# Kernel tuning notes

Measured on AMD Instinct MI355X. Metric: run time of the kernel, lower is better.

Reference implementation:

```python
import jax, jax.numpy as jnp
import numpy as np
from jax import lax

B_BLK = 16   # block size B
N_Z = 64     # latent dim


def setup_inputs() -> dict:
    key = jax.random.key(0)
    ks = jax.random.split(key, 6)
    in_ch, out_ch = 256, 256
    L = (out_ch // B_BLK) * (in_ch // B_BLK)  # 256 latent codes
    x = jax.random.normal(ks[0], (32, in_ch, 64, 64), dtype=jnp.float32)
    z = jax.random.normal(ks[1], (L, N_Z), dtype=jnp.float32)
    W1 = jax.random.normal(ks[2], (B_BLK, N_Z, N_Z), dtype=jnp.float32) * 0.1
    B1 = jax.random.normal(ks[3], (B_BLK, N_Z), dtype=jnp.float32) * 0.1
    W2 = jax.random.normal(ks[4], (B_BLK, B_BLK * 9, N_Z), dtype=jnp.float32) * 0.1
    B2 = jax.random.normal(ks[5], (B_BLK, B_BLK * 9), dtype=jnp.float32) * 0.1
    return {"x": x, "z": z, "W1": W1, "B1": B1, "W2": W2, "B2": B2}


def _aggregate_weight(z, W1, B1, W2, B2, out_ch, in_ch):
    # hypertype='separate', batched over all L = (out_ch//B)*(in_ch//B) blocks.
    # per block: a = W1 @ z + B1 -> (B, N_z); K = W2 @ a[...,None] + B2 -> (B, B*9)
    a = jnp.einsum('bdn,ln->lbd', W1, z) + B1            # (L, B, N_z)
    K = jnp.einsum('bkd,lbd->lbk', W2, a) + B2           # (L, B, B*9)
    ob, ib = out_ch // B_BLK, in_ch // B_BLK
    K = K.reshape(ob, ib, B_BLK, B_BLK, 3, 3)            # (o_blk, i_blk, b1, b2, 3, 3)
    # torch: K.reshape(B,B,3,3).permute(1,0,2,3) => weight_block[p,q] = K[q,p]
    # then cat over i_blk on dim 1 (in), over o_blk on dim 0 (out)
    w = K.transpose(0, 3, 1, 2, 4, 5)                    # (o_blk, b2, i_blk, b1, 3, 3)
    return w.reshape(out_ch, in_ch, 3, 3)


def reference(x, z, W1, B1, W2, B2):
    out_ch, in_ch = 256, 256
    weight = _aggregate_weight(z, W1, B1, W2, B2, out_ch, in_ch)
    # F.conv2d(x, weight, bias=None, stride=1, padding=kernel_size//2=1)
    return lax.conv_general_dilated(
        x, weight,
        window_strides=(1, 1),
        padding=[(1, 1), (1, 1)],
        dimension_numbers=('NCHW', 'OIHW', 'NCHW'))
```

## Files before the change

kernel.cpp:

```cpp
#include <hip/hip_runtime.h>

typedef unsigned short u16;
typedef unsigned int u32;
typedef __attribute__((ext_vector_type(8))) short short8;
typedef __attribute__((ext_vector_type(4))) float f32x4;

__device__ __forceinline__ u16 f2bf(float f) {
    u32 u = __float_as_uint(f);
    return (u16)((u + 0x7FFFu + ((u >> 16) & 1u)) >> 16);
}

#define COMP(f4, e) ((e) == 0 ? (f4).x : (e) == 1 ? (f4).y : (e) == 2 ? (f4).z : (f4).w)

__device__ __forceinline__ void gld16(const u16* g, u16* l) {
    __builtin_amdgcn_global_load_lds(
        (const __attribute__((address_space(1))) unsigned int*)(unsigned long long)(const void*)g,
        (__attribute__((address_space(3))) unsigned int*)(unsigned long long)(void*)l,
        16, 0, 0);
}

__global__ __launch_bounds__(256) void nchw2nhwc_pad(const float* __restrict__ x,
                                                     u16* __restrict__ xp) {
    __shared__ __align__(16) u16 T[64][264];
    const int tid = threadIdx.x;
    const int b   = blockIdx.x;
    const int n   = b >> 6;
    const int row = b & 63;
    const int g16 = tid >> 4;
    const int pxq = tid & 15;

    const float* src = x + ((size_t)n * 256 + g16 * 16) * 4096 + row * 64 + pxq * 4;
    float4 v[4][4];
#pragma unroll
    for (int u = 0; u < 4; ++u)
#pragma unroll
        for (int i = 0; i < 4; ++i)
            v[u][i] = *(const float4*)(src + (size_t)(u * 4 + i) * 4096);

#pragma unroll
    for (int u = 0; u < 4; ++u) {
        const int ic = g16 * 16 + u * 4;
#pragma unroll
        for (int e = 0; e < 4; ++e) {
            const int px = pxq * 4 + e;
            const u32 lo = ((u32)f2bf(COMP(v[u][1], e)) << 16) | f2bf(COMP(v[u][0], e));
            const u32 hi = ((u32)f2bf(COMP(v[u][3], e)) << 16) | f2bf(COMP(v[u][2], e));
            *(uint2*)&T[px][ic] = make_uint2(lo, hi);
        }
    }
    __syncthreads();

    const int c = tid & 31, p0 = tid >> 5;
    u16* dstN = xp + ((size_t)n * 4356 + (size_t)(row + 1) * 66 + 1) * 256 + c * 8;
#pragma unroll
    for (int pp = 0; pp < 8; ++pp) {
        const int px = pp * 8 + p0;
        *(uint4*)(dstN + (size_t)px * 256) = *(const uint4*)&T[px][c * 8];
    }

    u16* hrow = xp + ((size_t)n * 4356 + (size_t)(row + 1) * 66) * 256;
    if (tid < 64) {
        const int wp = (tid >> 5) ? 65 : 0;
        uint4 zz = {0u, 0u, 0u, 0u};
        *(uint4*)(hrow + (size_t)wp * 256 + (tid & 31) * 8) = zz;
    }
    if (row == 0) {
        u16* tb = xp + (size_t)n * 4356 * 256;
        uint4 zz = {0u, 0u, 0u, 0u};
        for (int i = tid; i < 2112; i += 256) *(uint4*)(tb + (size_t)i * 8) = zz;
    }
    if (row == 63) {
        u16* bb = xp + ((size_t)n * 4356 + 65 * 66) * 256;
        uint4 zz = {0u, 0u, 0u, 0u};
        for (int i = tid; i < 2112; i += 256) *(uint4*)(bb + (size_t)i * 8) = zz;
    }
}

__global__ __launch_bounds__(256) void wgen(const float* __restrict__ z,
                                            const float* __restrict__ W1,
                                            const float* __restrict__ B1,
                                            const float* __restrict__ W2,
                                            const float* __restrict__ B2,
                                            u16* __restrict__ wb) {
    __shared__ float zl[64][65];
    __shared__ float w1s[4096];
    __shared__ float aS[64][65];
    __shared__ float w2s[9216];

    const int tid = threadIdx.x;
    const int b   = blockIdx.x >> 2;
    const int lc  = blockIdx.x & 3;
    const int l   = tid & 63;
    const int g   = tid >> 6;

    const float* zg  = z  + (size_t)lc * 4096;
    const float* w1g = W1 + (size_t)b * 4096;
    const float* w2g = W2 + (size_t)b * 9216;
#pragma unroll
    for (int k = 0; k < 4; ++k) {
        const int i4 = tid + k * 256;
        const float4 v = *(const float4*)(zg + (size_t)i4 * 4);
        const int lr = i4 >> 4, nr = (i4 * 4) & 63;
        zl[lr][nr] = v.x; zl[lr][nr + 1] = v.y; zl[lr][nr + 2] = v.z; zl[lr][nr + 3] = v.w;
        *(float4*)(w1s + (size_t)i4 * 4) = *(const float4*)(w1g + (size_t)i4 * 4);
    }
#pragma unroll
    for (int k = 0; k < 9; ++k) {
        const int i4 = tid + k * 256;
        *(float4*)(w2s + (size_t)i4 * 4) = *(const float4*)(w2g + (size_t)i4 * 4);
    }
    __syncthreads();

    {
        float acc[16];
#pragma unroll
        for (int j = 0; j < 16; ++j) acc[j] = B1[b * 64 + g * 16 + j];
#pragma unroll
        for (int nb = 0; nb < 16; ++nb) {
            float zv0 = zl[l][nb * 4 + 0];
            float zv1 = zl[l][nb * 4 + 1];
            float zv2 = zl[l][nb * 4 + 2];
            float zv3 = zl[l][nb * 4 + 3];
#pragma unroll
            for (int j = 0; j < 16; ++j) {
                const float4 w = *(const float4*)(w1s + (g * 16 + j) * 64 + nb * 4);
                acc[j] += w.x * zv0 + w.y * zv1 + w.z * zv2 + w.w * zv3;
            }
        }
#pragma unroll
        for (int j = 0; j < 16; ++j) aS[l][g * 16 + j] = acc[j];
    }
    __syncthreads();

    float acc2[36];
#pragma unroll
    for (int t = 0; t < 36; ++t) acc2[t] = B2[b * 144 + g * 36 + t];
#pragma unroll
    for (int db = 0; db < 16; ++db) {
        float av0 = aS[l][db * 4 + 0];
        float av1 = aS[l][db * 4 + 1];
        float av2 = aS[l][db * 4 + 2];
        float av3 = aS[l][db * 4 + 3];
#pragma unroll
        for (int t = 0; t < 36; ++t) {
            const float4 w = *(const float4*)(w2s + (g * 36 + t) * 64 + db * 4);
            acc2[t] += w.x * av0 + w.y * av1 + w.z * av2 + w.w * av3;
        }
    }

    const int lg = lc * 64 + l;
    const int ob = lg >> 4, ib = lg & 15;
#pragma unroll
    for (int t = 0; t < 36; ++t) {
        const int b2 = 4 * g + t / 9;
        const int tap = t % 9;
        wb[(size_t)(ob * 16 + b2) * 2304 + tap * 256 + ib * 16 + b] = f2bf(acc2[t]);
    }
}

__global__ __launch_bounds__(256) void conv_mfma(const u16* __restrict__ xp,
                                                 const u16* __restrict__ wb,
                                                 float* __restrict__ out) {
    __shared__ __align__(16) u16 As[2][128 * 32];
    __shared__ __align__(16) u16 Bs[2][128 * 32];

    const int tid = threadIdx.x;
    const int b0  = blockIdx.x;
    const int bid = (b0 & 7) * 256 + (b0 >> 3);
    const int mt = bid & 1;
    const int nt = bid >> 1;
    const int n = nt >> 5;
    const int pimg = (nt & 31) << 7;
    const int oc0 = mt << 7;

    const int lane = tid & 63;
    const int wave = tid >> 6;
    const int wm = (wave >> 1) & 1, wn = wave & 1;
    const int lr = lane & 15, lq = lane >> 4;
    const int sw = (lq ^ (lr & 3)) * 8;

    const int ls = lane >> 2;
    const int swst = ((lane & 3) ^ (ls & 3)) * 8;
    const int rr0 = wave * 32 + ls;
    const int rr1 = rr0 + 16;
    const u16* wbA0 = wb + (size_t)(oc0 + rr0) * 2304 + swst;
    const u16* wbA1 = wb + (size_t)(oc0 + rr1) * 2304 + swst;
    const int p0 = pimg + rr0, p1 = pimg + rr1;
    const int pb0 = ((p0 >> 6) + 1) * 66 + (p0 & 63) + 1;
    const int pb1 = ((p1 >> 6) + 1) * 66 + (p1 & 63) + 1;
    const u16* xpN = xp + (size_t)n * 4356 * 256 + swst;

    auto stage = [&](int bi, int kt) {
        const int tap = kt >> 3, icb = kt & 7;
        const int t3 = tap / 3;
        const int dh = t3 - 1, dw = tap - t3 * 3 - 1;
        const int ko = tap * 256 + icb * 32;
        const int bo = (dh * 66 + dw) * 256 + icb * 32;
        u16* ab = &As[bi][wave * 1024];
        u16* bb = &Bs[bi][wave * 1024];
        gld16(wbA0 + ko, ab);
        gld16(wbA1 + ko, ab + 512);
        gld16(xpN + (pb0 * 256 + bo), bb);
        gld16(xpN + (pb1 * 256 + bo), bb + 512);
    };

    f32x4 acc[4][4];
    const f32x4 z4 = {0.f, 0.f, 0.f, 0.f};
#pragma unroll
    for (int i = 0; i < 4; ++i)
#pragma unroll
        for (int j = 0; j < 4; ++j) acc[i][j] = z4;

    stage(0, 0);
#pragma unroll 2
    for (int kt = 0; kt < 72; ++kt) {
        const int cur = kt & 1;
        __syncthreads();
        if (kt < 71) stage(cur ^ 1, kt + 1);

        const u16* Ab = &As[cur][0];
        const u16* Bb = &Bs[cur][0];
        short8 af[4], bf[4];
#pragma unroll
        for (int i = 0; i < 4; ++i) {
            af[i] = *(const short8*)(Ab + (wm * 64 + i * 16 + lr) * 32 + sw);
            bf[i] = *(const short8*)(Bb + (wn * 64 + i * 16 + lr) * 32 + sw);
        }
#pragma unroll
        for (int i = 0; i < 4; ++i)
#pragma unroll
            for (int j = 0; j < 4; ++j)
                acc[i][j] = __builtin_amdgcn_mfma_f32_16x16x32_bf16(
                    af[i], bf[j], acc[i][j], 0, 0, 0);
    }

    const size_t outn = (size_t)n * 256 * 4096;
#pragma unroll
    for (int i = 0; i < 4; ++i) {
        const int ocb = oc0 + wm * 64 + i * 16 + lq * 4;
#pragma unroll
        for (int j = 0; j < 4; ++j) {
            const int po = pimg + wn * 64 + j * 16 + lr;
            float* op = out + outn + (size_t)ocb * 4096 + po;
#pragma unroll
            for (int r = 0; r < 4; ++r) op[(size_t)r * 4096] = acc[i][j][r];
        }
    }
}

extern "C" void kernel_launch(void* const* d_in, const int* in_sizes, int n_in,
                              void* d_out, int out_size, void* d_ws, size_t ws_size,
                              hipStream_t stream) {
    const float* x  = (const float*)d_in[0];
    const float* z  = (const float*)d_in[1];
    const float* W1 = (const float*)d_in[2];
    const float* B1 = (const float*)d_in[3];
    const float* W2 = (const float*)d_in[4];
    const float* B2 = (const float*)d_in[5];
    float* out = (float*)d_out;

    u16* xp = (u16*)d_ws;
    u16* wb = xp + (size_t)32 * 4356 * 256;
    const size_t need = ((size_t)32 * 4356 * 256 + (size_t)256 * 2304) * 2;
    if (ws_size < need) return;

    nchw2nhwc_pad<<<dim3(2048), dim3(256), 0, stream>>>(x, xp);
    wgen<<<dim3(64), dim3(256), 0, stream>>>(z, W1, B1, W2, B2, wb);
    conv_mfma<<<dim3(2048), dim3(256), 0, stream>>>(xp, wb, out);
}
```

Baseline: 428.8 us.

## Enlarge conv tile to 256x256 with 4-stage async LDS pipeline

Each conv workgroup now computes all 256 output channels by 256 pixels using 8 waves, where before it computed a 128x128 tile. K-slices are staged through a 4-deep ring of LDS buffers with explicit vmcnt waits, replacing the double buffer and its per-step __syncthreads. MFMA issue is raised in priority with s_setprio. The bigger tile halves redundant global loads of weights and activations per FLOP and hides load latency better. In exchange it uses 128KB of LDS and 128 accumulator registers per lane, and launches only 512 blocks, which may hurt occupancy and tail balance.

```diff
diff --git a/kernel.cpp b/kernel.cpp
--- a/kernel.cpp
+++ b/kernel.cpp
@@ -158,92 +158,128 @@
     }
 }
 
-__global__ __launch_bounds__(256) void conv_mfma(const u16* __restrict__ xp,
-                                                 const u16* __restrict__ wb,
-                                                 float* __restrict__ out) {
-    __shared__ __align__(16) u16 As[2][128 * 32];
-    __shared__ __align__(16) u16 Bs[2][128 * 32];
-
-    const int tid = threadIdx.x;
-    const int b0  = blockIdx.x;
-    const int bid = (b0 & 7) * 256 + (b0 >> 3);
-    const int mt = bid & 1;
-    const int nt = bid >> 1;
-    const int n = nt >> 5;
-    const int pimg = (nt & 31) << 7;
-    const int oc0 = mt << 7;
-
+__global__ __launch_bounds__(512, 2) void conv_mfma(const u16* __restrict__ xp,
+                                                    const u16* __restrict__ wb,
+                                                    float* __restrict__ out) {
+    __shared__ __align__(16) u16 As[4][8192];
+    __shared__ __align__(16) u16 Bs[4][8192];
+
+    const int tid  = threadIdx.x;
+    const int b0   = blockIdx.x;
+    const int bid  = (b0 & 7) * 64 + (b0 >> 3);
+    const int n    = bid >> 4;
+    const int pimg = (bid & 15) << 8;
     const int lane = tid & 63;
     const int wave = tid >> 6;
-    const int wm = (wave >> 1) & 1, wn = wave & 1;
+    const int wm = wave >> 2;
+    const int wn = wave & 3;
     const int lr = lane & 15, lq = lane >> 4;
-    const int sw = (lq ^ (lr & 3)) * 8;
-
-    const int ls = lane >> 2;
-    const int swst = ((lane & 3) ^ (ls & 3)) * 8;
-    const int rr0 = wave * 32 + ls;
-    const int rr1 = rr0 + 16;
-    const u16* wbA0 = wb + (size_t)(oc0 + rr0) * 2304 + swst;
-    const u16* wbA1 = wb + (size_t)(oc0 + rr1) * 2304 + swst;
-    const int p0 = pimg + rr0, p1 = pimg + rr1;
-    const int pb0 = ((p0 >> 6) + 1) * 66 + (p0 & 63) + 1;
-    const int pb1 = ((p1 >> 6) + 1) * 66 + (p1 & 63) + 1;
-    const u16* xpN = xp + (size_t)n * 4356 * 256 + swst;
-
-    auto stage = [&](int bi, int kt) {
-        const int tap = kt >> 3, icb = kt & 7;
+
+    const int prw = tid >> 3;
+    const int psl = tid & 7;
+    const int sl  = psl ^ (prw & 7);
+    const int s4o = (sl & 3) * 8;
+    const int par = sl >> 2;
+    const int ocA0 = (prw)      * 2 + par;
+    const int ocA1 = (64 + prw) * 2 + par;
+    const u16* aG0 = wb + (size_t)ocA0 * 2304 + s4o;
+    const u16* aG1 = wb + (size_t)ocA1 * 2304 + s4o;
+    const int pxB0 = (prw)      * 2 + par;
+    const int pxB1 = (64 + prw) * 2 + par;
+    const int prow0 = (bid & 15) * 4;
+    const int pb0 = (prow0 + (pxB0 >> 6) + 1) * 66 + (pxB0 & 63) + 1;
+    const int pb1 = (prow0 + (pxB1 >> 6) + 1) * 66 + (pxB1 & 63) + 1;
+    const u16* xpN = xp + (size_t)n * 4356 * 256 + s4o;
+    const int ldst = wave * 512;
+
+    f32x4 acc[8][4];
+    const f32x4 z4 = {0.f, 0.f, 0.f, 0.f};
+#pragma unroll
+    for (int i = 0; i < 8; ++i)
+#pragma unroll
+        for (int j = 0; j < 4; ++j) acc[i][j] = z4;
+
+    auto stage = [&](int t) {
+        const int s = t & 3;
+        const int tap = t >> 3, icb = t & 7;
         const int t3 = tap / 3;
         const int dh = t3 - 1, dw = tap - t3 * 3 - 1;
         const int ko = tap * 256 + icb * 32;
         const int bo = (dh * 66 + dw) * 256 + icb * 32;
-        u16* ab = &As[bi][wave * 1024];
-        u16* bb = &Bs[bi][wave * 1024];
-        gld16(wbA0 + ko, ab);
-        gld16(wbA1 + ko, ab + 512);
-        gld16(xpN + (pb0 * 256 + bo), bb);
-        gld16(xpN + (pb1 * 256 + bo), bb + 512);
+        u16* as_ = &As[s][ldst];
+        u16* bs_ = &Bs[s][ldst];
+        gld16(aG0 + ko, as_);
+        gld16(aG1 + ko, as_ + 4096);
+        gld16(xpN + (pb0 * 256 + bo), bs_);
+        gld16(xpN + (pb1 * 256 + bo), bs_ + 4096);
     };
 
-    f32x4 acc[4][4];
-    const f32x4 z4 = {0.f, 0.f, 0.f, 0.f};
-#pragma unroll
-    for (int i = 0; i < 4; ++i)
-#pragma unroll
-        for (int j = 0; j < 4; ++j) acc[i][j] = z4;
-
-    stage(0, 0);
-#pragma unroll 2
-    for (int kt = 0; kt < 72; ++kt) {
-        const int cur = kt & 1;
-        __syncthreads();
-        if (kt < 71) stage(cur ^ 1, kt + 1);
-
-        const u16* Ab = &As[cur][0];
-        const u16* Bb = &Bs[cur][0];
-        short8 af[4], bf[4];
-#pragma unroll
-        for (int i = 0; i < 4; ++i) {
-            af[i] = *(const short8*)(Ab + (wm * 64 + i * 16 + lr) * 32 + sw);
-            bf[i] = *(const short8*)(Bb + (wn * 64 + i * 16 + lr) * 32 + sw);
-        }
-#pragma unroll
-        for (int i = 0; i < 4; ++i)
-#pragma unroll
-            for (int j = 0; j < 4; ++j)
-                acc[i][j] = __builtin_amdgcn_mfma_f32_16x16x32_bf16(
-                    af[i], bf[j], acc[i][j], 0, 0, 0);
-    }
+    auto compute = [&](int t) {
+        const int s = t & 3;
+        const u16* Ab = &As[s][0];
+        const u16* Bb = &Bs[s][0];
+        short8 bfr[4];
+#pragma unroll
+        for (int j = 0; j < 4; ++j) {
+            const int px = wn * 64 + j * 16 + lr;
+            const int pr = px >> 1;
+            const int ps = (((px & 1) << 2) | lq) ^ (pr & 7);
+            bfr[j] = *(const short8*)(Bb + pr * 64 + ps * 8);
+        }
+#pragma unroll
+        for (int mh = 0; mh < 2; ++mh) {
+            short8 afr[4];
+#pragma unroll
+            for (int i = 0; i < 4; ++i) {
+                const int oc = wm * 128 + mh * 64 + i * 16 + lr;
+                const int pr = oc >> 1;
+                const int ps = (((oc & 1) << 2) | lq) ^ (pr & 7);
+                afr[i] = *(const short8*)(Ab + pr * 64 + ps * 8);
+            }
+            __builtin_amdgcn_s_setprio(1);
+#pragma unroll
+            for (int i = 0; i < 4; ++i)
+#pragma unroll
+                for (int j = 0; j < 4; ++j)
+                    acc[mh * 4 + i][j] = __builtin_amdgcn_mfma_f32_16x16x32_bf16(
+                        afr[i], bfr[j], acc[mh * 4 + i][j], 0, 0, 0);
+            __builtin_amdgcn_s_setprio(0);
+        }
+    };
+
+    stage(0); stage(1); stage(2);
+
+#pragma unroll 1
+    for (int t = 0; t < 69; ++t) {
+        asm volatile("s_waitcnt vmcnt(8)" ::: "memory");
+        __builtin_amdgcn_s_barrier();
+        asm volatile("" ::: "memory");
+        compute(t);
+        stage(t + 3);
+    }
+    asm volatile("s_waitcnt vmcnt(8)" ::: "memory");
+    __builtin_amdgcn_s_barrier();
+    asm volatile("" ::: "memory");
+    compute(69);
+    asm volatile("s_waitcnt vmcnt(4)" ::: "memory");
+    __builtin_amdgcn_s_barrier();
+    asm volatile("" ::: "memory");
+    compute(70);
+    asm volatile("s_waitcnt vmcnt(0)" ::: "memory");
+    __builtin_amdgcn_s_barrier();
+    asm volatile("" ::: "memory");
+    compute(71);
 
     const size_t outn = (size_t)n * 256 * 4096;
 #pragma unroll
-    for (int i = 0; i < 4; ++i) {
-        const int ocb = oc0 + wm * 64 + i * 16 + lq * 4;
+    for (int mi = 0; mi < 8; ++mi) {
+        const int ocb = wm * 128 + mi * 16 + lq * 4;
 #pragma unroll
         for (int j = 0; j < 4; ++j) {
             const int po = pimg + wn * 64 + j * 16 + lr;
             float* op = out + outn + (size_t)ocb * 4096 + po;
 #pragma unroll
-            for (int r = 0; r < 4; ++r) op[(size_t)r * 4096] = acc[i][j][r];
+            for (int r = 0; r < 4; ++r) op[(size_t)r * 4096] = acc[mi][j][r];
         }
     }
 }
@@ -266,5 +302,5 @@
 
     nchw2nhwc_pad<<<dim3(2048), dim3(256), 0, stream>>>(x, xp);
     wgen<<<dim3(64), dim3(256), 0, stream>>>(z, W1, B1, W2, B2, wb);
-    conv_mfma<<<dim3(2048), dim3(256), 0, stream>>>(xp, wb, out);
-}
+    conv_mfma<<<dim3(512), dim3(512), 0, stream>>>(xp, wb, out);
+}
```

After: 392.7 us. -8.4%, faster.
